# Kernel optimization log

Measured on AMD Instinct MI355X. Metric: run time of the kernel, lower is better.

The kernel has to match this reference:

```python
import jax, jax.numpy as jnp
import numpy as np

N = 50000   # nodes
E = 600000  # edges
D = 128     # input_dim
H = 128     # hidden_dim
C = 1       # num_classes
EPS = 1e-5


def _glorot(key, fan_in, fan_out):
    s = (2.0 / (fan_in + fan_out)) ** 0.5
    return jax.random.normal(key, (fan_in, fan_out), jnp.float32) * s


def setup_inputs() -> dict:
    key = jax.random.key(0)
    ks = jax.random.split(key, 16)
    inp = {
        "x": jax.random.normal(ks[0], (N, D), jnp.float32),
        "edge_index": jax.random.randint(ks[1], (2, E), 0, N, dtype=jnp.int64),
        # GCN layer 0: D -> H, layers 1,2: H -> H
        "W0": _glorot(ks[2], D, H), "b0": jnp.zeros((H,), jnp.float32),
        "g0": jnp.ones((H,), jnp.float32), "be0": jnp.zeros((H,), jnp.float32),
        "W1": _glorot(ks[3], H, H), "b1": jnp.zeros((H,), jnp.float32),
        "g1": jnp.ones((H,), jnp.float32), "be1": jnp.zeros((H,), jnp.float32),
        "W2": _glorot(ks[4], H, H), "b2": jnp.zeros((H,), jnp.float32),
        "g2": jnp.ones((H,), jnp.float32), "be2": jnp.zeros((H,), jnp.float32),
        # MLP head: Linear(H,H) -> ReLU -> Linear(H,C)
        "hW1": _glorot(ks[5], H, H), "hb1": jnp.zeros((H,), jnp.float32),
        "hW2": _glorot(ks[6], H, C), "hb2": jnp.zeros((C,), jnp.float32),
    }
    return inp


def _layer_norm(h, g, b):
    mu = jnp.mean(h, axis=-1, keepdims=True)
    var = jnp.mean(jnp.square(h - mu), axis=-1, keepdims=True)
    return (h - mu) * jax.lax.rsqrt(var + EPS) * g + b


def reference(x, edge_index, W0, b0, g0, be0, W1, b1, g1, be1, W2, b2, g2, be2,
              hW1, hb1, hW2, hb2):
    # --- GCN normalization (add self-loops, symmetric deg^-1/2 norm) ---
    loop = jnp.arange(N, dtype=edge_index.dtype)
    src = jnp.concatenate([edge_index[0], loop])  # [E+N]
    dst = jnp.concatenate([edge_index[1], loop])  # [E+N]
    deg = jax.ops.segment_sum(jnp.ones_like(dst, jnp.float32), dst, num_segments=N)
    dinv = jax.lax.rsqrt(deg)  # deg >= 1 due to self-loops
    norm = (dinv[src] * dinv[dst])[:, None]  # [E+N, 1]

    def gcn_layer(h, W, b, g, be):
        hW = h @ W                                   # [N, H] dense GEMM
        msg = hW[src] * norm                         # gather + scale  [E+N, H]
        agg = jax.ops.segment_sum(msg, dst, num_segments=N) + b
        return jax.nn.relu(_layer_norm(agg, g, be))  # dropout = identity (eval)

    h = gcn_layer(x, W0, b0, g0, be0)
    h = gcn_layer(h, W1, b1, g1, be1)
    h = gcn_layer(h, W2, b2, g2, be2)

    # MLP head
    h = jax.nn.relu(h @ hW1 + hb1)
    logits = h @ hW2 + hb2  # [N, C]
    return logits
```

## Files before the change

kernel.cpp:

```cpp
#include <hip/hip_runtime.h>
#include <hip/hip_fp16.h>

#define N_NODES 50000
#define N_EDGES 600000
#define HDIM 128
#define EPS 1e-5f
#define ELLW 64

typedef __attribute__((ext_vector_type(4))) float f32x4;
typedef __attribute__((ext_vector_type(4))) _Float16 h16x4;
typedef __attribute__((ext_vector_type(8))) _Float16 h16x8;

#define EDGE_BLKS ((N_EDGES + 255) / 256)
#define CVT_BLKS 6250
#define PACK_BLKS 32

__global__ void detect_kernel(const int* __restrict__ ei, int* __restrict__ flag) {
    __shared__ int nonzero;
    if (threadIdx.x == 0) nonzero = 0;
    __syncthreads();
    int acc = 0;
    for (int i = threadIdx.x; i < 1024; i += blockDim.x)
        acc |= ei[2 * i + 1];
    if (acc) atomicOr(&nonzero, 1);
    __syncthreads();
    if (threadIdx.x == 0) *flag = (nonzero == 0) ? 1 : 0;
}

__device__ __forceinline__ int load_idx(const int* __restrict__ ei, int pos, int f) {
    return f ? ei[2 * pos] : ei[pos];
}

__device__ __forceinline__ void hsplit(float a, _Float16& hi, _Float16& lo) {
    _Float16 h = (_Float16)a;
    hi = h;
    lo = (_Float16)(a - (float)h);
}

__global__ void prep_kernel(const float* __restrict__ x, _Float16* __restrict__ xh,
                            const int* __restrict__ ei, const int* __restrict__ flag,
                            int* __restrict__ deg, unsigned short* __restrict__ ell,
                            const float* __restrict__ W0, const float* __restrict__ W1,
                            const float* __restrict__ W2, const float* __restrict__ W3,
                            _Float16* __restrict__ pkh, _Float16* __restrict__ pkl) {
    int b = blockIdx.x;
    if (b < EDGE_BLKS) {
        int e = b * 256 + threadIdx.x;
        if (e < N_EDGES) {
            int f = *flag;
            int s = load_idx(ei, e, f);
            int d = load_idx(ei, N_EDGES + e, f);
            int pos = atomicAdd(&deg[d], 1);
            if (pos < ELLW) ell[(size_t)d * ELLW + pos] = (unsigned short)s;
        }
    } else if (b < EDGE_BLKS + CVT_BLKS) {
        int idx = (b - EDGE_BLKS) * 256 + threadIdx.x;
        if (idx < N_NODES * 32) {
            float4 v = ((const float4*)x)[idx];
            h16x4 o;
            o[0] = (_Float16)v.x; o[1] = (_Float16)v.y;
            o[2] = (_Float16)v.z; o[3] = (_Float16)v.w;
            ((h16x4*)xh)[idx] = o;
        }
    } else {
        int pb = b - EDGE_BLKS - CVT_BLKS;
        int wsel = pb >> 3;
        const float* W = (wsel == 0) ? W0 : (wsel == 1) ? W1 : (wsel == 2) ? W2 : W3;
        int idx = (pb & 7) * 256 + threadIdx.x;
        int lane = idx & 63;
        int cf = (idx >> 6) & 7;
        int ks = idx >> 9;
        int col = cf * 16 + (lane & 15);
        int k0 = ks * 32 + (lane >> 4) * 8;
        _Float16 h[8], l[8];
#pragma unroll
        for (int i = 0; i < 8; ++i) hsplit(W[(size_t)(k0 + i) * HDIM + col], h[i], l[i]);
        size_t base = (size_t)wsel * 16384 + (size_t)idx * 8;
#pragma unroll
        for (int i = 0; i < 8; ++i) { pkh[base + i] = h[i]; pkl[base + i] = l[i]; }
    }
}

__global__ __launch_bounds__(256) void agg_kernel(const _Float16* __restrict__ h,
                                                  const int* __restrict__ deg,
                                                  const unsigned short* __restrict__ ell,
                                                  _Float16* __restrict__ out) {
    int node = blockIdx.x * 16 + (threadIdx.x >> 4);
    int sub = threadIdx.x & 15;
    if (node >= N_NODES) return;
    const h16x8* h8 = (const h16x8*)h;
    int dn = deg[node];
    float dd = rsqrtf((float)dn + 1.0f);
    h16x8 v = h8[(size_t)node * 16 + sub];
    float acc[8];
#pragma unroll
    for (int i = 0; i < 8; ++i) acc[i] = dd * (float)v[i];
    int cnt = min(dn, ELLW);
    const unsigned short* row = ell + (size_t)node * ELLW;
    for (int j = 0; j < cnt; j += 4) {
        uint2 pk = *(const uint2*)(row + j);
        int s0 = (int)(pk.x & 0xFFFFu);
        int s1 = (int)(pk.x >> 16);
        int s2 = (int)(pk.y & 0xFFFFu);
        int s3 = (int)(pk.y >> 16);
        bool k1 = j + 1 < cnt, k2 = j + 2 < cnt, k3 = j + 3 < cnt;
        s1 = k1 ? s1 : s0;
        s2 = k2 ? s2 : s0;
        s3 = k3 ? s3 : s0;
        int d0 = deg[s0];
        int d1 = deg[s1];
        int d2 = deg[s2];
        int d3 = deg[s3];
        h16x8 u0 = h8[(size_t)s0 * 16 + sub];
        h16x8 u1 = h8[(size_t)s1 * 16 + sub];
        h16x8 u2 = h8[(size_t)s2 * 16 + sub];
        h16x8 u3 = h8[(size_t)s3 * 16 + sub];
        float w0 = rsqrtf((float)d0 + 1.0f);
        float w1 = k1 ? rsqrtf((float)d1 + 1.0f) : 0.f;
        float w2 = k2 ? rsqrtf((float)d2 + 1.0f) : 0.f;
        float w3 = k3 ? rsqrtf((float)d3 + 1.0f) : 0.f;
#pragma unroll
        for (int i = 0; i < 8; ++i) {
            acc[i] += w0 * (float)u0[i];
            acc[i] += w1 * (float)u1[i];
            acc[i] += w2 * (float)u2[i];
            acc[i] += w3 * (float)u3[i];
        }
    }
    h16x8 r;
#pragma unroll
    for (int i = 0; i < 8; ++i) r[i] = (_Float16)(acc[i] * dd);
    ((h16x8*)out)[(size_t)node * 16 + sub] = r;
}

__global__ __launch_bounds__(256) void gemm_mfma(const _Float16* __restrict__ A,
                                                 const _Float16* __restrict__ Bh,
                                                 const _Float16* __restrict__ Bl,
                                                 const float* __restrict__ bias,
                                                 const float* __restrict__ gamma,
                                                 const float* __restrict__ beta,
                                                 void* __restrict__ outraw,
                                                 int mode, int nrows) {
    int t = threadIdx.x;
    int wave = t >> 6, lane = t & 63;
    int lrow = lane & 15, lk = lane >> 4;
    int rowb = blockIdx.x * 64 + wave * 16;

    f32x4 acc[8];
#pragma unroll
    for (int cf = 0; cf < 8; ++cf) acc[cf] = (f32x4){0.f, 0.f, 0.f, 0.f};

    const _Float16* arow = A + (size_t)(rowb + lrow) * HDIM;

#pragma unroll
    for (int ks = 0; ks < 4; ++ks) {
        h16x8 a = *(const h16x8*)(arow + ks * 32 + lk * 8);
        const _Float16* bhp = Bh + (size_t)(ks * 8) * 512 + (size_t)lane * 8;
        const _Float16* blp = Bl + (size_t)(ks * 8) * 512 + (size_t)lane * 8;
#pragma unroll
        for (int cf = 0; cf < 8; ++cf) {
            h16x8 bh = *(const h16x8*)(bhp + (size_t)cf * 512);
            h16x8 bl = *(const h16x8*)(blp + (size_t)cf * 512);
            acc[cf] = __builtin_amdgcn_mfma_f32_16x16x32_f16(a, bh, acc[cf], 0, 0, 0);
            acc[cf] = __builtin_amdgcn_mfma_f32_16x16x32_f16(a, bl, acc[cf], 0, 0, 0);
        }
    }

    float bias_v[8];
#pragma unroll
    for (int cf = 0; cf < 8; ++cf) bias_v[cf] = bias[cf * 16 + lrow];

    if (mode == 0) {
        _Float16* out = (_Float16*)outraw;
        float gam[8], bet[8];
#pragma unroll
        for (int cf = 0; cf < 8; ++cf) {
            gam[cf] = gamma[cf * 16 + lrow];
            bet[cf] = beta[cf * 16 + lrow];
        }
#pragma unroll
        for (int r = 0; r < 4; ++r) {
            float vv[8];
            float s1 = 0.f;
#pragma unroll
            for (int cf = 0; cf < 8; ++cf) {
                vv[cf] = acc[cf][r] + bias_v[cf];
                s1 += vv[cf];
            }
#pragma unroll
            for (int m = 1; m <= 8; m <<= 1) s1 += __shfl_xor(s1, m);
            float mean = s1 * (1.0f / 128.0f);
            float s2 = 0.f;
            float cc[8];
#pragma unroll
            for (int cf = 0; cf < 8; ++cf) {
                cc[cf] = vv[cf] - mean;
                s2 += cc[cf] * cc[cf];
            }
#pragma unroll
            for (int m = 1; m <= 8; m <<= 1) s2 += __shfl_xor(s2, m);
            float var = s2 * (1.0f / 128.0f);
            float rs = rsqrtf(var + EPS);
            int row = rowb + lk * 4 + r;
            if (row < nrows) {
#pragma unroll
                for (int cf = 0; cf < 8; ++cf) {
                    float y = cc[cf] * rs * gam[cf] + bet[cf];
                    out[(size_t)row * HDIM + cf * 16 + lrow] = (_Float16)(y > 0.f ? y : 0.f);
                }
            }
        }
    } else {
        float* out = (float*)outraw;
        float w2v[8];
#pragma unroll
        for (int cf = 0; cf < 8; ++cf) w2v[cf] = gamma[cf * 16 + lrow];
        float b2 = beta[0];
#pragma unroll
        for (int r = 0; r < 4; ++r) {
            float part = 0.f;
#pragma unroll
            for (int cf = 0; cf < 8; ++cf) {
                float y = acc[cf][r] + bias_v[cf];
                y = y > 0.f ? y : 0.f;
                part += y * w2v[cf];
            }
#pragma unroll
            for (int m = 1; m <= 8; m <<= 1) part += __shfl_xor(part, m);
            int row = rowb + lk * 4 + r;
            if (row < nrows && lrow == 0) out[row] = part + b2;
        }
    }
}

extern "C" void kernel_launch(void* const* d_in, const int* in_sizes, int n_in,
                              void* d_out, int out_size, void* d_ws, size_t ws_size,
                              hipStream_t stream) {
    (void)in_sizes; (void)n_in; (void)out_size; (void)ws_size;
    const float* x   = (const float*)d_in[0];
    const int*   ei  = (const int*)d_in[1];
    const float* W0  = (const float*)d_in[2];
    const float* b0  = (const float*)d_in[3];
    const float* g0  = (const float*)d_in[4];
    const float* be0 = (const float*)d_in[5];
    const float* W1  = (const float*)d_in[6];
    const float* b1  = (const float*)d_in[7];
    const float* g1  = (const float*)d_in[8];
    const float* be1 = (const float*)d_in[9];
    const float* W2  = (const float*)d_in[10];
    const float* b2  = (const float*)d_in[11];
    const float* g2  = (const float*)d_in[12];
    const float* be2 = (const float*)d_in[13];
    const float* hW1 = (const float*)d_in[14];
    const float* hb1 = (const float*)d_in[15];
    const float* hW2 = (const float*)d_in[16];
    const float* hb2 = (const float*)d_in[17];
    float* out = (float*)d_out;

    char* w = (char*)d_ws;
    size_t off = 0;
    auto alloc = [&](size_t bytes) -> void* {
        void* p = w + off;
        off += (bytes + 255) & ~(size_t)255;
        return p;
    };
    int*            deg  = (int*)alloc((size_t)N_NODES * 4);
    unsigned short* ell  = (unsigned short*)alloc((size_t)N_NODES * ELLW * 2);
    int*            flag = (int*)alloc(256);
    _Float16*       hagg = (_Float16*)alloc((size_t)N_NODES * HDIM * 2);
    _Float16*       xh   = (_Float16*)alloc((size_t)N_NODES * HDIM * 2);
    _Float16*       hA   = (_Float16*)alloc((size_t)N_NODES * HDIM * 2);
    _Float16*       hB   = (_Float16*)alloc((size_t)N_NODES * HDIM * 2);
    _Float16*       pkh  = (_Float16*)alloc((size_t)4 * 16384 * 2);
    _Float16*       pkl  = (_Float16*)alloc((size_t)4 * 16384 * 2);

    hipMemsetAsync(deg, 0, (size_t)N_NODES * 4, stream);

    detect_kernel<<<1, 256, 0, stream>>>(ei, flag);
    prep_kernel<<<EDGE_BLKS + CVT_BLKS + PACK_BLKS, 256, 0, stream>>>(
        x, xh, ei, flag, deg, ell, W0, W1, W2, hW1, pkh, pkl);

    int nab = (N_NODES + 15) / 16;
    int ngb = (N_NODES + 63) / 64;
    agg_kernel<<<nab, 256, 0, stream>>>(xh, deg, ell, hagg);
    gemm_mfma<<<ngb, 256, 0, stream>>>(hagg, pkh, pkl, b0, g0, be0, hA, 0, N_NODES);
    agg_kernel<<<nab, 256, 0, stream>>>(hA, deg, ell, hagg);
    gemm_mfma<<<ngb, 256, 0, stream>>>(hagg, pkh + (size_t)16384, pkl + (size_t)16384,
                                       b1, g1, be1, hB, 0, N_NODES);
    agg_kernel<<<nab, 256, 0, stream>>>(hB, deg, ell, hagg);
    gemm_mfma<<<ngb, 256, 0, stream>>>(hagg, pkh + (size_t)2 * 16384, pkl + (size_t)2 * 16384,
                                       b2, g2, be2, hA, 0, N_NODES);
    gemm_mfma<<<ngb, 256, 0, stream>>>(hA, pkh + (size_t)3 * 16384, pkl + (size_t)3 * 16384,
                                       hb1, hW2, hb2, out, 1, N_NODES);
}
```

Before: 184.5 us.

## Fuse neighbor aggregation into MFMA GEMM+LayerNorm kernel per GCN layer

Merges the separate aggregation and GEMM kernels into one kernel per layer. Each block aggregates 64 nodes into a padded shared-memory tile, then runs the split-fp16 MFMA GEMM with LayerNorm/ReLU directly from LDS. This removes the hagg intermediate round trip through global memory and three kernel launches. In exchange, aggregation parallelism drops from 16-node blocks to 64-node blocks, with each thread looping over 4 nodes, which may lower latency hiding for the irregular gathers.

After: 172.2 us. 1.07x faster.

```diff
diff --git a/kernel.cpp b/kernel.cpp
--- a/kernel.cpp
+++ b/kernel.cpp
@@ -6,6 +6,7 @@
 #define HDIM 128
 #define EPS 1e-5f
 #define ELLW 64
+#define LPADH 136
 
 typedef __attribute__((ext_vector_type(4))) float f32x4;
 typedef __attribute__((ext_vector_type(4))) _Float16 h16x4;
@@ -81,66 +82,146 @@
     }
 }
 
-__global__ __launch_bounds__(256) void agg_kernel(const _Float16* __restrict__ h,
-                                                  const int* __restrict__ deg,
-                                                  const unsigned short* __restrict__ ell,
-                                                  _Float16* __restrict__ out) {
-    int node = blockIdx.x * 16 + (threadIdx.x >> 4);
-    int sub = threadIdx.x & 15;
-    if (node >= N_NODES) return;
-    const h16x8* h8 = (const h16x8*)h;
-    int dn = deg[node];
-    float dd = rsqrtf((float)dn + 1.0f);
-    h16x8 v = h8[(size_t)node * 16 + sub];
-    float acc[8];
-#pragma unroll
-    for (int i = 0; i < 8; ++i) acc[i] = dd * (float)v[i];
-    int cnt = min(dn, ELLW);
-    const unsigned short* row = ell + (size_t)node * ELLW;
-    for (int j = 0; j < cnt; j += 4) {
-        uint2 pk = *(const uint2*)(row + j);
-        int s0 = (int)(pk.x & 0xFFFFu);
-        int s1 = (int)(pk.x >> 16);
-        int s2 = (int)(pk.y & 0xFFFFu);
-        int s3 = (int)(pk.y >> 16);
-        bool k1 = j + 1 < cnt, k2 = j + 2 < cnt, k3 = j + 3 < cnt;
-        s1 = k1 ? s1 : s0;
-        s2 = k2 ? s2 : s0;
-        s3 = k3 ? s3 : s0;
-        int d0 = deg[s0];
-        int d1 = deg[s1];
-        int d2 = deg[s2];
-        int d3 = deg[s3];
-        h16x8 u0 = h8[(size_t)s0 * 16 + sub];
-        h16x8 u1 = h8[(size_t)s1 * 16 + sub];
-        h16x8 u2 = h8[(size_t)s2 * 16 + sub];
-        h16x8 u3 = h8[(size_t)s3 * 16 + sub];
-        float w0 = rsqrtf((float)d0 + 1.0f);
-        float w1 = k1 ? rsqrtf((float)d1 + 1.0f) : 0.f;
-        float w2 = k2 ? rsqrtf((float)d2 + 1.0f) : 0.f;
-        float w3 = k3 ? rsqrtf((float)d3 + 1.0f) : 0.f;
-#pragma unroll
-        for (int i = 0; i < 8; ++i) {
-            acc[i] += w0 * (float)u0[i];
-            acc[i] += w1 * (float)u1[i];
-            acc[i] += w2 * (float)u2[i];
-            acc[i] += w3 * (float)u3[i];
-        }
-    }
-    h16x8 r;
-#pragma unroll
-    for (int i = 0; i < 8; ++i) r[i] = (_Float16)(acc[i] * dd);
-    ((h16x8*)out)[(size_t)node * 16 + sub] = r;
-}
-
-__global__ __launch_bounds__(256) void gemm_mfma(const _Float16* __restrict__ A,
+__global__ __launch_bounds__(256) void layer_fused(const _Float16* __restrict__ h,
+                                                   const int* __restrict__ deg,
+                                                   const unsigned short* __restrict__ ell,
+                                                   const _Float16* __restrict__ Bh,
+                                                   const _Float16* __restrict__ Bl,
+                                                   const float* __restrict__ bias,
+                                                   const float* __restrict__ gamma,
+                                                   const float* __restrict__ beta,
+                                                   _Float16* __restrict__ out, int nrows) {
+    __shared__ _Float16 As[64][LPADH];
+    int t = threadIdx.x;
+    int blockRow = blockIdx.x * 64;
+
+    {
+        int g = t >> 4, sub = t & 15;
+        const h16x8* h8 = (const h16x8*)h;
+        for (int j = 0; j < 4; ++j) {
+            int rl = j * 16 + g;
+            int node = blockRow + rl;
+            h16x8 r;
+            if (node < nrows) {
+                int dn = deg[node];
+                float dd = rsqrtf((float)dn + 1.0f);
+                h16x8 v = h8[(size_t)node * 16 + sub];
+                float acc[8];
+#pragma unroll
+                for (int i = 0; i < 8; ++i) acc[i] = dd * (float)v[i];
+                int cnt = min(dn, ELLW);
+                const unsigned short* row = ell + (size_t)node * ELLW;
+                for (int e = 0; e < cnt; e += 4) {
+                    uint2 pk = *(const uint2*)(row + e);
+                    int s0 = (int)(pk.x & 0xFFFFu);
+                    int s1 = (int)(pk.x >> 16);
+                    int s2 = (int)(pk.y & 0xFFFFu);
+                    int s3 = (int)(pk.y >> 16);
+                    bool k1 = e + 1 < cnt, k2 = e + 2 < cnt, k3 = e + 3 < cnt;
+                    s1 = k1 ? s1 : s0;
+                    s2 = k2 ? s2 : s0;
+                    s3 = k3 ? s3 : s0;
+                    int d0 = deg[s0];
+                    int d1 = deg[s1];
+                    int d2 = deg[s2];
+                    int d3 = deg[s3];
+                    h16x8 u0 = h8[(size_t)s0 * 16 + sub];
+                    h16x8 u1 = h8[(size_t)s1 * 16 + sub];
+                    h16x8 u2 = h8[(size_t)s2 * 16 + sub];
+                    h16x8 u3 = h8[(size_t)s3 * 16 + sub];
+                    float w0 = rsqrtf((float)d0 + 1.0f);
+                    float w1 = k1 ? rsqrtf((float)d1 + 1.0f) : 0.f;
+                    float w2 = k2 ? rsqrtf((float)d2 + 1.0f) : 0.f;
+                    float w3 = k3 ? rsqrtf((float)d3 + 1.0f) : 0.f;
+#pragma unroll
+                    for (int i = 0; i < 8; ++i) {
+                        acc[i] += w0 * (float)u0[i];
+                        acc[i] += w1 * (float)u1[i];
+                        acc[i] += w2 * (float)u2[i];
+                        acc[i] += w3 * (float)u3[i];
+                    }
+                }
+#pragma unroll
+                for (int i = 0; i < 8; ++i) r[i] = (_Float16)(acc[i] * dd);
+            } else {
+#pragma unroll
+                for (int i = 0; i < 8; ++i) r[i] = (_Float16)0.f;
+            }
+            *(h16x8*)&As[rl][sub * 8] = r;
+        }
+    }
+    __syncthreads();
+
+    int wave = t >> 6, lane = t & 63;
+    int lrow = lane & 15, lk = lane >> 4;
+    int rowb = blockRow + wave * 16;
+
+    f32x4 acc[8];
+#pragma unroll
+    for (int cf = 0; cf < 8; ++cf) acc[cf] = (f32x4){0.f, 0.f, 0.f, 0.f};
+
+#pragma unroll
+    for (int ks = 0; ks < 4; ++ks) {
+        h16x8 a = *(const h16x8*)&As[wave * 16 + lrow][ks * 32 + lk * 8];
+        const _Float16* bhp = Bh + (size_t)(ks * 8) * 512 + (size_t)lane * 8;
+        const _Float16* blp = Bl + (size_t)(ks * 8) * 512 + (size_t)lane * 8;
+#pragma unroll
+        for (int cf = 0; cf < 8; ++cf) {
+            h16x8 bh = *(const h16x8*)(bhp + (size_t)cf * 512);
+            h16x8 bl = *(const h16x8*)(blp + (size_t)cf * 512);
+            acc[cf] = __builtin_amdgcn_mfma_f32_16x16x32_f16(a, bh, acc[cf], 0, 0, 0);
+            acc[cf] = __builtin_amdgcn_mfma_f32_16x16x32_f16(a, bl, acc[cf], 0, 0, 0);
+        }
+    }
+
+    float bias_v[8], gam[8], bet[8];
+#pragma unroll
+    for (int cf = 0; cf < 8; ++cf) {
+        bias_v[cf] = bias[cf * 16 + lrow];
+        gam[cf] = gamma[cf * 16 + lrow];
+        bet[cf] = beta[cf * 16 + lrow];
+    }
+#pragma unroll
+    for (int r = 0; r < 4; ++r) {
+        float vv[8];
+        float s1 = 0.f;
+#pragma unroll
+        for (int cf = 0; cf < 8; ++cf) {
+            vv[cf] = acc[cf][r] + bias_v[cf];
+            s1 += vv[cf];
+        }
+#pragma unroll
+        for (int m = 1; m <= 8; m <<= 1) s1 += __shfl_xor(s1, m);
+        float mean = s1 * (1.0f / 128.0f);
+        float s2 = 0.f;
+        float cc[8];
+#pragma unroll
+        for (int cf = 0; cf < 8; ++cf) {
+            cc[cf] = vv[cf] - mean;
+            s2 += cc[cf] * cc[cf];
+        }
+#pragma unroll
+        for (int m = 1; m <= 8; m <<= 1) s2 += __shfl_xor(s2, m);
+        float var = s2 * (1.0f / 128.0f);
+        float rs = rsqrtf(var + EPS);
+        int row = rowb + lk * 4 + r;
+        if (row < nrows) {
+#pragma unroll
+            for (int cf = 0; cf < 8; ++cf) {
+                float y = cc[cf] * rs * gam[cf] + bet[cf];
+                out[(size_t)row * HDIM + cf * 16 + lrow] = (_Float16)(y > 0.f ? y : 0.f);
+            }
+        }
+    }
+}
+
+__global__ __launch_bounds__(256) void head_mfma(const _Float16* __restrict__ A,
                                                  const _Float16* __restrict__ Bh,
                                                  const _Float16* __restrict__ Bl,
                                                  const float* __restrict__ bias,
-                                                 const float* __restrict__ gamma,
-                                                 const float* __restrict__ beta,
-                                                 void* __restrict__ outraw,
-                                                 int mode, int nrows) {
+                                                 const float* __restrict__ w2,
+                                                 const float* __restrict__ b2p,
+                                                 float* __restrict__ out, int nrows) {
     int t = threadIdx.x;
     int wave = t >> 6, lane = t & 63;
     int lrow = lane & 15, lk = lane >> 4;
@@ -151,7 +232,6 @@
     for (int cf = 0; cf < 8; ++cf) acc[cf] = (f32x4){0.f, 0.f, 0.f, 0.f};
 
     const _Float16* arow = A + (size_t)(rowb + lrow) * HDIM;
-
 #pragma unroll
     for (int ks = 0; ks < 4; ++ks) {
         h16x8 a = *(const h16x8*)(arow + ks * 32 + lk * 8);
@@ -166,70 +246,26 @@
         }
     }
 
-    float bias_v[8];
-#pragma unroll
-    for (int cf = 0; cf < 8; ++cf) bias_v[cf] = bias[cf * 16 + lrow];
-
-    if (mode == 0) {
-        _Float16* out = (_Float16*)outraw;
-        float gam[8], bet[8];
-#pragma unroll
-        for (int cf = 0; cf < 8; ++cf) {
-            gam[cf] = gamma[cf * 16 + lrow];
-            bet[cf] = beta[cf * 16 + lrow];
-        }
-#pragma unroll
-        for (int r = 0; r < 4; ++r) {
-            float vv[8];
-            float s1 = 0.f;
-#pragma unroll
-            for (int cf = 0; cf < 8; ++cf) {
-                vv[cf] = acc[cf][r] + bias_v[cf];
-                s1 += vv[cf];
-            }
-#pragma unroll
-            for (int m = 1; m <= 8; m <<= 1) s1 += __shfl_xor(s1, m);
-            float mean = s1 * (1.0f / 128.0f);
-            float s2 = 0.f;
-            float cc[8];
-#pragma unroll
-            for (int cf = 0; cf < 8; ++cf) {
-                cc[cf] = vv[cf] - mean;
-                s2 += cc[cf] * cc[cf];
-            }
-#pragma unroll
-            for (int m = 1; m <= 8; m <<= 1) s2 += __shfl_xor(s2, m);
-            float var = s2 * (1.0f / 128.0f);
-            float rs = rsqrtf(var + EPS);
-            int row = rowb + lk * 4 + r;
-            if (row < nrows) {
-#pragma unroll
-                for (int cf = 0; cf < 8; ++cf) {
-                    float y = cc[cf] * rs * gam[cf] + bet[cf];
-                    out[(size_t)row * HDIM + cf * 16 + lrow] = (_Float16)(y > 0.f ? y : 0.f);
-                }
-            }
-        }
-    } else {
-        float* out = (float*)outraw;
-        float w2v[8];
-#pragma unroll
-        for (int cf = 0; cf < 8; ++cf) w2v[cf] = gamma[cf * 16 + lrow];
-        float b2 = beta[0];
-#pragma unroll
-        for (int r = 0; r < 4; ++r) {
-            float part = 0.f;
-#pragma unroll
-            for (int cf = 0; cf < 8; ++cf) {
-                float y = acc[cf][r] + bias_v[cf];
-                y = y > 0.f ? y : 0.f;
-                part += y * w2v[cf];
-            }
-#pragma unroll
-            for (int m = 1; m <= 8; m <<= 1) part += __shfl_xor(part, m);
-            int row = rowb + lk * 4 + r;
-            if (row < nrows && lrow == 0) out[row] = part + b2;
-        }
+    float bias_v[8], w2v[8];
+#pragma unroll
+    for (int cf = 0; cf < 8; ++cf) {
+        bias_v[cf] = bias[cf * 16 + lrow];
+        w2v[cf] = w2[cf * 16 + lrow];
+    }
+    float b2 = b2p[0];
+#pragma unroll
+    for (int r = 0; r < 4; ++r) {
+        float part = 0.f;
+#pragma unroll
+        for (int cf = 0; cf < 8; ++cf) {
+            float y = acc[cf][r] + bias_v[cf];
+            y = y > 0.f ? y : 0.f;
+            part += y * w2v[cf];
+        }
+#pragma unroll
+        for (int m = 1; m <= 8; m <<= 1) part += __shfl_xor(part, m);
+        int row = rowb + lk * 4 + r;
+        if (row < nrows && lrow == 0) out[row] = part + b2;
     }
 }
 
@@ -267,7 +303,6 @@
     int*            deg  = (int*)alloc((size_t)N_NODES * 4);
     unsigned short* ell  = (unsigned short*)alloc((size_t)N_NODES * ELLW * 2);
     int*            flag = (int*)alloc(256);
-    _Float16*       hagg = (_Float16*)alloc((size_t)N_NODES * HDIM * 2);
     _Float16*       xh   = (_Float16*)alloc((size_t)N_NODES * HDIM * 2);
     _Float16*       hA   = (_Float16*)alloc((size_t)N_NODES * HDIM * 2);
     _Float16*       hB   = (_Float16*)alloc((size_t)N_NODES * HDIM * 2);
@@ -280,16 +315,12 @@
     prep_kernel<<<EDGE_BLKS + CVT_BLKS + PACK_BLKS, 256, 0, stream>>>(
         x, xh, ei, flag, deg, ell, W0, W1, W2, hW1, pkh, pkl);
 
-    int nab = (N_NODES + 15) / 16;
     int ngb = (N_NODES + 63) / 64;
-    agg_kernel<<<nab, 256, 0, stream>>>(xh, deg, ell, hagg);
-    gemm_mfma<<<ngb, 256, 0, stream>>>(hagg, pkh, pkl, b0, g0, be0, hA, 0, N_NODES);
-    agg_kernel<<<nab, 256, 0, stream>>>(hA, deg, ell, hagg);
-    gemm_mfma<<<ngb, 256, 0, stream>>>(hagg, pkh + (size_t)16384, pkl + (size_t)16384,
-                                       b1, g1, be1, hB, 0, N_NODES);
-    agg_kernel<<<nab, 256, 0, stream>>>(hB, deg, ell, hagg);
-    gemm_mfma<<<ngb, 256, 0, stream>>>(hagg, pkh + (size_t)2 * 16384, pkl + (size_t)2 * 16384,
-                                       b2, g2, be2, hA, 0, N_NODES);
-    gemm_mfma<<<ngb, 256, 0, stream>>>(hA, pkh + (size_t)3 * 16384, pkl + (size_t)3 * 16384,
-                                       hb1, hW2, hb2, out, 1, N_NODES);
-}
+    layer_fused<<<ngb, 256, 0, stream>>>(xh, deg, ell, pkh, pkl, b0, g0, be0, hA, N_NODES);
+    layer_fused<<<ngb, 256, 0, stream>>>(hA, deg, ell, pkh + (size_t)16384, pkl + (size_t)16384,
+                                         b1, g1, be1, hB, N_NODES);
+    layer_fused<<<ngb, 256, 0, stream>>>(hB, deg, ell, pkh + (size_t)2 * 16384, pkl + (size_t)2 * 16384,
+                                         b2, g2, be2, hA, N_NODES);
+    head_mfma<<<ngb, 256, 0, stream>>>(hA, pkh + (size_t)3 * 16384, pkl + (size_t)3 * 16384,
+                                       hb1, hW2, hb2, out, N_NODES);
+}
```
